# Optimization experiments

Measured on AMD Instinct MI355X. Metric: run time of the kernel, lower is better.

Reference implementation:

```python
import jax, jax.numpy as jnp
import numpy as np

N, E, B = 50000, 800000, 128
F_IN, F_MID, HEADS = 78, 156, 2

def setup_inputs() -> dict:
    key = jax.random.key(0)
    ks = jax.random.split(key, 20)
    s = 0.05
    x = jax.random.normal(ks[0], (N, F_IN), dtype=jnp.float32)
    edge_index = jax.random.randint(ks[1], (2, E), 0, N, dtype=jnp.int64)
    batch = jnp.sort(jax.random.randint(ks[2], (N,), 0, B, dtype=jnp.int64))
    return {
        'x': x, 'edge_index': edge_index, 'batch': batch,
        'W1': jax.random.normal(ks[3], (F_IN, F_MID), jnp.float32) * s,
        'b1': jnp.zeros((F_MID,), jnp.float32),
        'W2': jax.random.normal(ks[4], (F_MID, HEADS * F_MID), jnp.float32) * s,
        'att_src': jax.random.normal(ks[5], (HEADS, F_MID), jnp.float32) * s,
        'att_dst': jax.random.normal(ks[6], (HEADS, F_MID), jnp.float32) * s,
        'b2': jnp.zeros((HEADS * F_MID,), jnp.float32),
        'Wg': jax.random.normal(ks[7], (HEADS * F_MID, 128), jnp.float32) * s,
        'bg': jnp.zeros((128,), jnp.float32),
        'Wf1': jax.random.normal(ks[8], (128, 1024), jnp.float32) * s,
        'bf1': jnp.zeros((1024,), jnp.float32),
        'Wf2': jax.random.normal(ks[9], (1024, 512), jnp.float32) * s,
        'bf2': jnp.zeros((512,), jnp.float32),
        'Wo': jax.random.normal(ks[10], (512, 1), jnp.float32) * s,
        'bo': jnp.zeros((1,), jnp.float32),
    }

def _forward(x, edge_index, batch, W1, b1, W2, att_src, att_dst, b2,
             Wg, bg, Wf1, bf1, Wf2, bf2, Wo, bo):
    n = x.shape[0]
    loop = jnp.arange(n, dtype=edge_index.dtype)
    src = jnp.concatenate([edge_index[0], loop])  # with self-loops (PyG default)
    dst = jnp.concatenate([edge_index[1], loop])

    # ---- GCNConv: D^{-1/2}(A+I)D^{-1/2} X W + b ----
    h = x @ W1                                            # [N,156]
    deg = jax.ops.segment_sum(jnp.ones_like(dst, jnp.float32), dst, num_segments=n)
    dinv = jnp.where(deg > 0, jax.lax.rsqrt(jnp.maximum(deg, 1.0)), 0.0)
    norm = dinv[src] * dinv[dst]                          # [E+N]
    h = jax.ops.segment_sum(h[src] * norm[:, None], dst, num_segments=n) + b1
    h = jax.nn.leaky_relu(h, 0.01)                        # self.activation

    # ---- GATConv (heads=2, concat) ----
    g = (h @ W2).reshape(n, HEADS, F_MID)                 # [N,H,F]
    a_src = jnp.einsum('nhf,hf->nh', g, att_src)          # [N,H]
    a_dst = jnp.einsum('nhf,hf->nh', g, att_dst)
    e = jax.nn.leaky_relu(a_src[src] + a_dst[dst], 0.2)   # [E+N,H]
    m = jax.ops.segment_max(e, dst, num_segments=n)       # per-dst softmax
    alpha = jnp.exp(e - m[dst])
    denom = jax.ops.segment_sum(alpha, dst, num_segments=n)
    alpha = alpha / denom[dst]
    g = jax.ops.segment_sum(g[src] * alpha[:, :, None], dst, num_segments=n)
    g = g.reshape(n, HEADS * F_MID) + b2
    g = jax.nn.leaky_relu(g, 0.01)

    # ---- global max pool over graphs ----
    p = jax.ops.segment_max(g, batch, num_segments=B)     # [B,312]

    p = jax.nn.leaky_relu(p @ Wg + bg, 0.01)              # fc_g1 + activation
    p = jax.nn.relu(p @ Wf1 + bf1)                        # fc1
    p = jax.nn.relu(p @ Wf2 + bf2)                        # fc2
    return p @ Wo + bo                                    # out [B,1]

def reference(x, edge_index, batch, W1, b1, W2, att_src, att_dst, b2,
              Wg, bg, Wf1, bf1, Wf2, bf2, Wo, bo):
    return _forward(x, edge_index, batch, W1, b1, W2, att_src, att_dst, b2,
                    Wg, bg, Wf1, bf1, Wf2, bf2, Wo, bo)
```

## Files before the change

kernel.cpp:

```cpp
#include <hip/hip_runtime.h>
#include <cstdint>
#include <cstddef>

#define F_INP 78
#define F_MID 156
#define C2    312
#define GDIM  128
#define F1D   1024
#define F2D   512

#define NEG_SENTINEL -1e30f
#define SCAN_BLOCKS 256

typedef _Float16 half_t;
typedef _Float16 half8 __attribute__((ext_vector_type(8)));
typedef float f32x4 __attribute__((ext_vector_type(4)));

__device__ __forceinline__ float leaky(float v, float s) { return v > 0.f ? v : s * v; }
__device__ __forceinline__ int rfl(int v) { return __builtin_amdgcn_readfirstlane(v); }


__global__ void deg_count_kernel(const int* __restrict__ ei, int* __restrict__ deg, int E) {
    int e = blockIdx.x * blockDim.x + threadIdx.x;
    if (e >= E) return;
    atomicAdd(&deg[ei[E + e]], 1);
}

__global__ void scan_p1_kernel(const int* __restrict__ deg, int* __restrict__ partials, int N) {
    __shared__ int red[256];
    int b = blockIdx.x, t = threadIdx.x;
    int chunk = (N + SCAN_BLOCKS - 1) / SCAN_BLOCKS;
    int start = b * chunk;
    int end = start + chunk; if (end > N) end = N;
    int s = 0;
    for (int i = start + t; i < end; i += 256) s += deg[i];
    red[t] = s;
    __syncthreads();
    for (int off = 128; off; off >>= 1) {
        if (t < off) red[t] += red[t + off];
        __syncthreads();
    }
    if (t == 0) partials[b] = red[0];
}

__global__ void scan_p2_kernel(int* __restrict__ partials) {
    __shared__ int s[SCAN_BLOCKS];
    int t = threadIdx.x;
    s[t] = partials[t];
    __syncthreads();
    for (int off = 1; off < SCAN_BLOCKS; off <<= 1) {
        int v = (t >= off) ? s[t - off] : 0;
        __syncthreads();
        s[t] += v;
        __syncthreads();
    }
    partials[t] = (t == 0) ? 0 : s[t - 1];
}

__global__ void scan_p3_kernel(const int* __restrict__ deg, const int* __restrict__ partials,
                               int* __restrict__ row_ptr, int* __restrict__ cursor,
                               float* __restrict__ dinv, int N, int E) {
    __shared__ int red[256];
    int b = blockIdx.x, t = threadIdx.x;
    int chunk = (N + SCAN_BLOCKS - 1) / SCAN_BLOCKS;
    int start = b * chunk;
    int end = start + chunk; if (end > N) end = N;
    int sub = (chunk + 255) / 256;
    int ts = start + t * sub;
    int te = ts + sub; if (te > end) te = end; if (ts > end) ts = end;
    int s = 0;
    for (int i = ts; i < te; i++) s += deg[i];
    red[t] = s;
    __syncthreads();
    for (int off = 1; off < 256; off <<= 1) {
        int v = (t >= off) ? red[t - off] : 0;
        __syncthreads();
        red[t] += v;
        __syncthreads();
    }
    int run = partials[b] + ((t == 0) ? 0 : red[t - 1]);
    for (int i = ts; i < te; i++) {
        int dg = deg[i];
        row_ptr[i] = run;
        cursor[i] = run;
        dinv[i] = rsqrtf((float)dg + 1.0f);
        run += dg;
    }
    if (b == 0 && t == 0) row_ptr[N] = E;
}

__global__ void fill_csr_kernel(const int* __restrict__ ei, int* __restrict__ cursor,
                                int* __restrict__ col, int E) {
    int e = blockIdx.x * blockDim.x + threadIdx.x;
    if (e >= E) return;
    int s = ei[e], d = ei[E + e];
    int pos = atomicAdd(&cursor[d], 1);
    col[pos] = s;
}


__global__ void lin1_kernel(const float* __restrict__ x, const float* __restrict__ W1,
                            const float* __restrict__ dinv, half_t* __restrict__ h_lin, int N) {
    __shared__ float2 xs[16][39];
    int tid = threadIdx.x;
    int n0 = blockIdx.x * 16;
    const float2* x2 = (const float2*)x;
    for (int i = tid; i < 16 * 39; i += 192) {
        int r = i / 39, c = i % 39;
        int n = n0 + r;
        float2 z; z.x = 0.f; z.y = 0.f;
        if (n < N) {
            float dn = dinv[n];
            float2 v = x2[(size_t)n * 39 + c];
            z.x = v.x * dn; z.y = v.y * dn;
        }
        xs[r][c] = z;
    }
    __syncthreads();
    if (tid >= 160) return;
    if (tid >= F_MID) {
        for (int r = 0; r < 16; r++) {
            int n = n0 + r;
            if (n < N) h_lin[(size_t)n * 160 + tid] = (half_t)0.f;
        }
        return;
    }
    float acc[16] = {};
    for (int k2 = 0; k2 < 39; k2++) {
        float w0 = W1[(2 * k2) * F_MID + tid];
        float w1 = W1[(2 * k2 + 1) * F_MID + tid];
        #pragma unroll
        for (int r = 0; r < 16; r++) {
            float2 xv = xs[r][k2];
            acc[r] += xv.x * w0 + xv.y * w1;
        }
    }
    #pragma unroll
    for (int r = 0; r < 16; r++) {
        int n = n0 + r;
        if (n < N) h_lin[(size_t)n * 160 + tid] = (half_t)acc[r];
    }
}

__global__ void w2t_kernel(const float* __restrict__ W2, half_t* __restrict__ w2t) {
    int idx = blockIdx.x * blockDim.x + threadIdx.x;
    if (idx >= 320 * 160) return;
    int coln = idx / 160, k = idx % 160;
    float v = (coln < C2 && k < F_MID) ? W2[k * C2 + coln] : 0.f;
    w2t[idx] = (half_t)v;
}

__global__ void wT_kernel(const float* __restrict__ Wg, const float* __restrict__ Wf1,
                          const float* __restrict__ Wf2, float* __restrict__ wgT,
                          float* __restrict__ wf1T, float* __restrict__ wf2T) {
    int idx = blockIdx.x * blockDim.x + threadIdx.x;
    if (idx < GDIM * C2) {
        int c = idx / C2, k = idx % C2;
        wgT[idx] = Wg[k * GDIM + c];
        return;
    }
    idx -= GDIM * C2;
    if (idx < F1D * GDIM) {
        int c = idx / GDIM, k = idx % GDIM;
        wf1T[idx] = Wf1[k * F1D + c];
        return;
    }
    idx -= F1D * GDIM;
    if (idx < F2D * F1D) {
        int c = idx / F1D, k = idx % F1D;
        wf2T[idx] = Wf2[k * F2D + c];
    }
}

__global__ void lin2_mfma_kernel(const half_t* __restrict__ h16, const half_t* __restrict__ w2t,
                                 half_t* __restrict__ g, int N) {
    int wid  = (blockIdx.x * blockDim.x + threadIdx.x) >> 6;
    int lane = threadIdx.x & 63;
    int m0 = wid * 32;
    if (m0 >= N) return;
    int rl = lane & 15;
    int kg = lane >> 4;
    bool has2 = (m0 + 16) < N;

    const half8* hv = (const half8*)h16;
    const half8* wv = (const half8*)w2t;
    half8 zz = {(half_t)0.f,(half_t)0.f,(half_t)0.f,(half_t)0.f,
                (half_t)0.f,(half_t)0.f,(half_t)0.f,(half_t)0.f};

    half8 a0[5], a1[5];
    size_t rA = (size_t)(m0 + rl) * 20;
    size_t rB = (size_t)(m0 + 16 + rl) * 20;
    #pragma unroll
    for (int ks = 0; ks < 5; ks++) {
        a0[ks] = hv[rA + ks * 4 + kg];
        a1[ks] = has2 ? hv[rB + ks * 4 + kg] : zz;
    }

    for (int n0 = 0; n0 < 20; n0++) {
        f32x4 c0 = {0.f, 0.f, 0.f, 0.f};
        f32x4 c1 = {0.f, 0.f, 0.f, 0.f};
        size_t wb = (size_t)(n0 * 16 + rl) * 20 + kg;
        #pragma unroll
        for (int ks = 0; ks < 5; ks++) {
            half8 b = wv[wb + ks * 4];
            c0 = __builtin_amdgcn_mfma_f32_16x16x32_f16(a0[ks], b, c0, 0, 0, 0);
            c1 = __builtin_amdgcn_mfma_f32_16x16x32_f16(a1[ks], b, c1, 0, 0, 0);
        }
        int col = n0 * 16 + rl;
        if (col < C2) {
            int r0 = kg * 4;
            #pragma unroll
            for (int j = 0; j < 4; j++) {
                g[(size_t)(m0 + r0 + j) * C2 + col] = (half_t)c0[j];
            }
            if (has2) {
                #pragma unroll
                for (int j = 0; j < 4; j++) {
                    g[(size_t)(m0 + 16 + r0 + j) * C2 + col] = (half_t)c1[j];
                }
            }
        }
    }
}

__global__ void gcn_gather_kernel(const half_t* __restrict__ h_lin, const int* __restrict__ row_ptr,
                                  const int* __restrict__ col, const float* __restrict__ dinv,
                                  const float* __restrict__ b1, half_t* __restrict__ h16, int N) {
    int wid  = (blockIdx.x * blockDim.x + threadIdx.x) >> 6;
    int lane = threadIdx.x & 63;
    if (wid >= N) return;
    int d  = wid;
    int jb = row_ptr[d], je = row_ptr[d + 1];
    float dd = dinv[d];
    const half8* h8v = (const half8*)h_lin;
    bool actv = lane < 20;
    int f0 = lane * 8;
    float acc[8] = {};
    if (actv) {
        half8 v = h8v[(size_t)d * 20 + lane];
        #pragma unroll
        for (int e = 0; e < 8; e++) acc[e] = (float)v[e];
    }
    int j = jb;
    for (; j + 3 < je; j += 4) {
        int s0 = rfl(col[j]);
        int s1 = rfl(col[j + 1]);
        int s2 = rfl(col[j + 2]);
        int s3 = rfl(col[j + 3]);
        if (actv) {
            half8 v0 = h8v[(size_t)s0 * 20 + lane];
            half8 v1 = h8v[(size_t)s1 * 20 + lane];
            half8 v2 = h8v[(size_t)s2 * 20 + lane];
            half8 v3 = h8v[(size_t)s3 * 20 + lane];
            #pragma unroll
            for (int e = 0; e < 8; e++)
                acc[e] += (float)v0[e] + (float)v1[e] + (float)v2[e] + (float)v3[e];
        }
    }
    for (; j < je; j++) {
        int s = rfl(col[j]);
        if (actv) {
            half8 v = h8v[(size_t)s * 20 + lane];
            #pragma unroll
            for (int e = 0; e < 8; e++) acc[e] += (float)v[e];
        }
    }
    if (actv) {
        half8 o;
        #pragma unroll
        for (int e = 0; e < 8; e++) {
            int f = f0 + e;
            float val = 0.f;
            if (f < F_MID) val = leaky(dd * acc[e] + b1[f], 0.01f);
            o[e] = (half_t)val;
        }
        ((half8*)h16)[(size_t)d * 20 + lane] = o;
    }
}

__global__ void att_kernel(const half_t* __restrict__ g, const float* __restrict__ att_src,
                           const float* __restrict__ att_dst, float2* __restrict__ a_src,
                           float2* __restrict__ a_dst, int N) {
    int wid  = (blockIdx.x * blockDim.x + threadIdx.x) >> 6;
    int lane = threadIdx.x & 63;
    if (wid >= N) return;
    const half8* g8 = (const half8*)g;
    float vs0 = 0.f, vs1 = 0.f, vd0 = 0.f, vd1 = 0.f;
    if (lane < 39) {
        half8 v = g8[(size_t)wid * 39 + lane];
        int f0 = lane * 8;
        #pragma unroll
        for (int e = 0; e < 8; e++) {
            int f = f0 + e;
            float gv = (float)v[e];
            float sw = att_src[f];
            float dw = att_dst[f];
            if (f < F_MID) { vs0 += gv * sw; vd0 += gv * dw; }
            else           { vs1 += gv * sw; vd1 += gv * dw; }
        }
    }
    #pragma unroll
    for (int off = 32; off; off >>= 1) {
        vs0 += __shfl_xor(vs0, off);
        vs1 += __shfl_xor(vs1, off);
        vd0 += __shfl_xor(vd0, off);
        vd1 += __shfl_xor(vd1, off);
    }
    if (lane == 0) {
        float2 s; s.x = vs0; s.y = vs1;
        float2 t; t.x = vd0; t.y = vd1;
        a_src[wid] = s;
        a_dst[wid] = t;
    }
}

__global__ void gat_msw_kernel(const float2* __restrict__ a_src, const float2* __restrict__ a_dst,
                               const int* __restrict__ row_ptr, const int* __restrict__ col,
                               float4* __restrict__ minv, float2* __restrict__ wbuf, int N) {
    int wid  = (blockIdx.x * blockDim.x + threadIdx.x) >> 6;
    int lane = threadIdx.x & 63;
    if (wid >= N) return;
    int d  = wid;
    int jb = row_ptr[d], je = row_ptr[d + 1];
    float2 ad = a_dst[d];
    float2 asd = a_src[d];
    float es0 = leaky(asd.x + ad.x, 0.2f);
    float es1 = leaky(asd.y + ad.y, 0.2f);

    float m0 = NEG_SENTINEL, s0 = 0.f, m1 = NEG_SENTINEL, s1 = 0.f;
    for (int j = jb + lane; j < je; j += 64) {
        float2 as = a_src[col[j]];
        float e0 = leaky(as.x + ad.x, 0.2f);
        float e1 = leaky(as.y + ad.y, 0.2f);
        float nm0 = fmaxf(m0, e0); s0 = s0 * __expf(m0 - nm0) + __expf(e0 - nm0); m0 = nm0;
        float nm1 = fmaxf(m1, e1); s1 = s1 * __expf(m1 - nm1) + __expf(e1 - nm1); m1 = nm1;
    }
    #pragma unroll
    for (int off = 32; off; off >>= 1) {
        float om0 = __shfl_xor(m0, off), os0 = __shfl_xor(s0, off);
        float om1 = __shfl_xor(m1, off), os1 = __shfl_xor(s1, off);
        float nm0 = fmaxf(m0, om0);
        s0 = s0 * __expf(m0 - nm0) + os0 * __expf(om0 - nm0); m0 = nm0;
        float nm1 = fmaxf(m1, om1);
        s1 = s1 * __expf(m1 - nm1) + os1 * __expf(om1 - nm1); m1 = nm1;
    }
    {
        float nm0 = fmaxf(m0, es0);
        s0 = s0 * __expf(m0 - nm0) + __expf(es0 - nm0); m0 = nm0;
        float nm1 = fmaxf(m1, es1);
        s1 = s1 * __expf(m1 - nm1) + __expf(es1 - nm1); m1 = nm1;
    }
    float i0 = 1.0f / s0, i1 = 1.0f / s1;
    if (lane == 0) {
        float4 r; r.x = m0; r.y = i0; r.z = m1; r.w = i1;
        minv[d] = r;
    }
    for (int j = jb + lane; j < je; j += 64) {
        float2 as = a_src[col[j]];
        float2 w;
        w.x = __expf(leaky(as.x + ad.x, 0.2f) - m0) * i0;
        w.y = __expf(leaky(as.y + ad.y, 0.2f) - m1) * i1;
        wbuf[j] = w;
    }
}

__global__ void gat_gather_kernel(const half_t* __restrict__ g, const float2* __restrict__ a_src,
                                  const float2* __restrict__ a_dst, const int* __restrict__ row_ptr,
                                  const int* __restrict__ col, const float2* __restrict__ wbuf,
                                  const float4* __restrict__ minv, float* __restrict__ gout, int N) {
    int wid  = (blockIdx.x * blockDim.x + threadIdx.x) >> 6;
    int lane = threadIdx.x & 63;
    if (wid >= N) return;
    int d  = wid;
    int jb = row_ptr[d], je = row_ptr[d + 1];
    const half8* g8 = (const half8*)g;
    bool actv = lane < 39;
    int f0 = lane * 8;
    bool lo0 = f0 < F_MID;
    bool hi0 = (f0 + 4) < F_MID;
    float acc[8] = {};
    {
        float2 ad = a_dst[d];
        float2 asd = a_src[d];
        float4 mv = minv[d];
        float w0 = __expf(leaky(asd.x + ad.x, 0.2f) - mv.x) * mv.y;
        float w1 = __expf(leaky(asd.y + ad.y, 0.2f) - mv.z) * mv.w;
        if (actv) {
            half8 v = g8[(size_t)d * 39 + lane];
            float wlo = lo0 ? w0 : w1;
            float whi = hi0 ? w0 : w1;
            #pragma unroll
            for (int e = 0; e < 4; e++) acc[e] = (float)v[e] * wlo;
            #pragma unroll
            for (int e = 4; e < 8; e++) acc[e] = (float)v[e] * whi;
        }
    }
    int j = jb;
    for (; j + 3 < je; j += 4) {
        int s0 = rfl(col[j]);
        int s1 = rfl(col[j + 1]);
        int s2 = rfl(col[j + 2]);
        int s3 = rfl(col[j + 3]);
        float2 W0 = wbuf[j], W1v = wbuf[j + 1], W2v = wbuf[j + 2], W3v = wbuf[j + 3];
        if (actv) {
            half8 v0 = g8[(size_t)s0 * 39 + lane];
            half8 v1 = g8[(size_t)s1 * 39 + lane];
            half8 v2 = g8[(size_t)s2 * 39 + lane];
            half8 v3 = g8[(size_t)s3 * 39 + lane];
            float a0 = lo0 ? W0.x : W0.y,  b0 = hi0 ? W0.x : W0.y;
            float a1 = lo0 ? W1v.x : W1v.y, b1 = hi0 ? W1v.x : W1v.y;
            float a2 = lo0 ? W2v.x : W2v.y, b2 = hi0 ? W2v.x : W2v.y;
            float a3 = lo0 ? W3v.x : W3v.y, b3 = hi0 ? W3v.x : W3v.y;
            #pragma unroll
            for (int e = 0; e < 4; e++)
                acc[e] += (float)v0[e] * a0 + (float)v1[e] * a1 + (float)v2[e] * a2 + (float)v3[e] * a3;
            #pragma unroll
            for (int e = 4; e < 8; e++)
                acc[e] += (float)v0[e] * b0 + (float)v1[e] * b1 + (float)v2[e] * b2 + (float)v3[e] * b3;
        }
    }
    for (; j < je; j++) {
        int s = rfl(col[j]);
        float2 w2 = wbuf[j];
        if (actv) {
            half8 v = g8[(size_t)s * 39 + lane];
            float wlo = lo0 ? w2.x : w2.y;
            float whi = hi0 ? w2.x : w2.y;
            #pragma unroll
            for (int e = 0; e < 4; e++) acc[e] += (float)v[e] * wlo;
            #pragma unroll
            for (int e = 4; e < 8; e++) acc[e] += (float)v[e] * whi;
        }
    }
    if (actv) {
        float* orow = gout + (size_t)d * C2 + f0;
        float4 o0; o0.x = acc[0]; o0.y = acc[1]; o0.z = acc[2]; o0.w = acc[3];
        float4 o1; o1.x = acc[4]; o1.y = acc[5]; o1.z = acc[6]; o1.w = acc[7];
        *(float4*)orow = o0;
        *(float4*)(orow + 4) = o1;
    }
}


__global__ void starts_kernel(const int* __restrict__ batch, int* __restrict__ starts, int N, int B) {
    int b = blockIdx.x * blockDim.x + threadIdx.x;
    if (b > B) return;
    if (b == B) { starts[B] = N; return; }
    int lo = 0, hi = N;
    while (lo < hi) {
        int mid = (lo + hi) >> 1;
        if (batch[mid] < b) lo = mid + 1; else hi = mid;
    }
    starts[b] = lo;
}

__global__ void pool_kernel(const float* __restrict__ gout, const float* __restrict__ b2,
                            const int* __restrict__ starts, float* __restrict__ p0) {
    int b = blockIdx.x;
    int t = threadIdx.x;
    if (t >= 78) return;
    int s = starts[b], e = starts[b + 1];
    const float4* g4 = (const float4*)gout;
    float4 m0, m1, m2, m3;
    m0.x = m0.y = m0.z = m0.w = -INFINITY;
    m1 = m0; m2 = m0; m3 = m0;
    int n = s;
    for (; n + 3 < e; n += 4) {
        float4 v0 = g4[(size_t)(n + 0) * 78 + t];
        float4 v1 = g4[(size_t)(n + 1) * 78 + t];
        float4 v2 = g4[(size_t)(n + 2) * 78 + t];
        float4 v3 = g4[(size_t)(n + 3) * 78 + t];
        m0.x = fmaxf(m0.x, v0.x); m0.y = fmaxf(m0.y, v0.y); m0.z = fmaxf(m0.z, v0.z); m0.w = fmaxf(m0.w, v0.w);
        m1.x = fmaxf(m1.x, v1.x); m1.y = fmaxf(m1.y, v1.y); m1.z = fmaxf(m1.z, v1.z); m1.w = fmaxf(m1.w, v1.w);
        m2.x = fmaxf(m2.x, v2.x); m2.y = fmaxf(m2.y, v2.y); m2.z = fmaxf(m2.z, v2.z); m2.w = fmaxf(m2.w, v2.w);
        m3.x = fmaxf(m3.x, v3.x); m3.y = fmaxf(m3.y, v3.y); m3.z = fmaxf(m3.z, v3.z); m3.w = fmaxf(m3.w, v3.w);
    }
    for (; n < e; n++) {
        float4 v = g4[(size_t)n * 78 + t];
        m0.x = fmaxf(m0.x, v.x); m0.y = fmaxf(m0.y, v.y); m0.z = fmaxf(m0.z, v.z); m0.w = fmaxf(m0.w, v.w);
    }
    m0.x = fmaxf(fmaxf(m0.x, m1.x), fmaxf(m2.x, m3.x));
    m0.y = fmaxf(fmaxf(m0.y, m1.y), fmaxf(m2.y, m3.y));
    m0.z = fmaxf(fmaxf(m0.z, m1.z), fmaxf(m2.z, m3.z));
    m0.w = fmaxf(fmaxf(m0.w, m1.w), fmaxf(m2.w, m3.w));
    float4 bb = ((const float4*)b2)[t];
    float4 o;
    o.x = leaky(m0.x + bb.x, 0.01f);
    o.y = leaky(m0.y + bb.y, 0.01f);
    o.z = leaky(m0.z + bb.z, 0.01f);
    o.w = leaky(m0.w + bb.w, 0.01f);
    ((float4*)p0)[(size_t)b * 78 + t] = o;
}

template <int KDIM, int ACT>
__global__ void fcT_kernel(const float* __restrict__ in, const float* __restrict__ Wt,
                           const float* __restrict__ bias, float* __restrict__ out,
                           int Bn, int OUT) {
    int wid  = (blockIdx.x * blockDim.x + threadIdx.x) >> 6;
    int lane = threadIdx.x & 63;
    if (wid >= Bn * OUT) return;
    int b = wid / OUT, c = wid % OUT;
    const float* irow = in + (size_t)b * KDIM;
    const float* wrow = Wt + (size_t)c * KDIM;
    float acc = 0.f;
    #pragma unroll 4
    for (int k = lane; k < KDIM; k += 64)
        acc += irow[k] * wrow[k];
    #pragma unroll
    for (int off = 32; off; off >>= 1) acc += __shfl_xor(acc, off);
    if (lane == 0) {
        acc += bias[c];
        if (ACT == 1) acc = leaky(acc, 0.01f);
        if (ACT == 2) acc = fmaxf(acc, 0.f);
        out[wid] = acc;
    }
}

extern "C" void kernel_launch(void* const* d_in, const int* in_sizes, int n_in,
                              void* d_out, int out_size, void* d_ws, size_t ws_size,
                              hipStream_t stream) {
    const float* x       = (const float*)d_in[0];
    const int*   ei      = (const int*)d_in[1];
    const int*   batch   = (const int*)d_in[2];
    const float* W1      = (const float*)d_in[3];
    const float* b1      = (const float*)d_in[4];
    const float* W2      = (const float*)d_in[5];
    const float* att_src = (const float*)d_in[6];
    const float* att_dst = (const float*)d_in[7];
    const float* b2      = (const float*)d_in[8];
    const float* Wg      = (const float*)d_in[9];
    const float* bg      = (const float*)d_in[10];
    const float* Wf1     = (const float*)d_in[11];
    const float* bf1     = (const float*)d_in[12];
    const float* Wf2     = (const float*)d_in[13];
    const float* bf2     = (const float*)d_in[14];
    const float* Wo      = (const float*)d_in[15];
    const float* bo      = (const float*)d_in[16];
    float* out = (float*)d_out;

    const int N  = in_sizes[0] / F_INP;
    const int E  = in_sizes[1] / 2;
    const int Bn = out_size;

    char* base = (char*)d_ws;
    size_t off = 0;
    auto take = [&](size_t bytes) -> void* {
        off = (off + 15) & ~(size_t)15;
        void* p = base + off;
        off += bytes;
        return p;
    };
    half_t* g      = (half_t*)take((size_t)C2 * N * 2);
    char*   AA     = (char*)take((size_t)C2 * N * 4);
    half_t* h_lin  = (half_t*)AA;
    half_t* h16    = (half_t*)(AA + (size_t)160 * N * 2);
    float*  gout   = (float*)AA;
    half_t* w2t    = (half_t*)take((size_t)320 * 160 * 2);
    float*  wgT    = (float*)take((size_t)GDIM * C2 * 4);
    float*  wf1T   = (float*)take((size_t)F1D * GDIM * 4);
    float*  wf2T   = (float*)take((size_t)F2D * F1D * 4);
    float4* minv   = (float4*)take((size_t)N * 16);
    float2* a_src  = (float2*)take((size_t)N * 8);
    float2* a_dst  = (float2*)take((size_t)N * 8);
    float2* wbuf   = (float2*)take((size_t)E * 8);
    float*  dinv   = (float*)take((size_t)N * 4);
    int*    deg_i  = (int*)take((size_t)N * 4);
    int*    partials = (int*)take((size_t)SCAN_BLOCKS * 4);
    int*    row_ptr= (int*)take((size_t)(N + 1) * 4);
    int*    cursor = (int*)take((size_t)N * 4);
    int*    col    = (int*)take((size_t)E * 4);
    int*    starts = (int*)take((size_t)(Bn + 1) * 4);
    float*  p0     = (float*)take((size_t)Bn * C2 * 4);
    float*  p1     = (float*)take((size_t)Bn * GDIM * 4);
    float*  p2     = (float*)take((size_t)Bn * F1D * 4);
    float*  p3     = (float*)take((size_t)Bn * F2D * 4);

    hipMemsetAsync(deg_i, 0, (size_t)N * sizeof(int), stream);

    starts_kernel<<<1, 256, 0, stream>>>(batch, starts, N, Bn);
    w2t_kernel<<<(320 * 160 + 255) / 256, 256, 0, stream>>>(W2, w2t);
    {
        int tot = GDIM * C2 + F1D * GDIM + F2D * F1D;
        wT_kernel<<<(tot + 255) / 256, 256, 0, stream>>>(Wg, Wf1, Wf2, wgT, wf1T, wf2T);
    }

    deg_count_kernel<<<(E + 255) / 256, 256, 0, stream>>>(ei, deg_i, E);
    scan_p1_kernel<<<SCAN_BLOCKS, 256, 0, stream>>>(deg_i, partials, N);
    scan_p2_kernel<<<1, SCAN_BLOCKS, 0, stream>>>(partials);
    scan_p3_kernel<<<SCAN_BLOCKS, 256, 0, stream>>>(deg_i, partials, row_ptr, cursor, dinv, N, E);
    fill_csr_kernel<<<(E + 255) / 256, 256, 0, stream>>>(ei, cursor, col, E);

    lin1_kernel<<<(N + 15) / 16, 192, 0, stream>>>(x, W1, dinv, h_lin, N);
    gcn_gather_kernel<<<(N + 3) / 4, 256, 0, stream>>>(h_lin, row_ptr, col, dinv, b1, h16, N);

    {
        int mwaves = (N + 31) / 32;
        int blocks = (mwaves + 3) / 4;
        lin2_mfma_kernel<<<blocks, 256, 0, stream>>>(h16, w2t, g, N);
    }
    att_kernel<<<(N + 3) / 4, 256, 0, stream>>>(g, att_src, att_dst, a_src, a_dst, N);
    gat_msw_kernel<<<(N + 3) / 4, 256, 0, stream>>>(a_src, a_dst, row_ptr, col, minv, wbuf, N);
    gat_gather_kernel<<<(N + 3) / 4, 256, 0, stream>>>(g, a_src, a_dst, row_ptr, col, wbuf, minv, gout, N);

    pool_kernel<<<Bn, 128, 0, stream>>>(gout, b2, starts, p0);
    {
        auto blocks_for = [](int waves) { return (waves + 3) / 4; };
        fcT_kernel<C2, 1><<<blocks_for(Bn * GDIM), 256, 0, stream>>>(p0, wgT, bg, p1, Bn, GDIM);
        fcT_kernel<GDIM, 2><<<blocks_for(Bn * F1D), 256, 0, stream>>>(p1, wf1T, bf1, p2, Bn, F1D);
        fcT_kernel<F1D, 2><<<blocks_for(Bn * F2D), 256, 0, stream>>>(p2, wf2T, bf2, p3, Bn, F2D);
        fcT_kernel<F2D, 0><<<blocks_for(Bn), 256, 0, stream>>>(p3, Wo, bo, out, Bn, 1);
    }
}
```

Measured before the change: 537.8 us.

## Use MFMA for first linear layer and store GAT output in fp16

Replaces the scalar fp32 lin1 kernel with a pre-pass that scales x by dinv and converts it to padded fp16, a transposed fp16 W1, and an MFMA 16x16x32 GEMM. Separately, the GAT gather output is now written as fp16 instead of fp32, and the pooling kernel reads half8 vectors, halving the traffic between those two kernels. In exchange it adds two extra launches and reduced precision in x and the pooled input. The MFMA kernel reads rows up to m0+31 of hx without a full tail guard, which could run out of bounds when N is not a multiple of 32; N=50000 is a multiple of 16 but not of 32.

Result: faster. 508.2 us (-5.5%).

```diff
diff --git a/kernel.cpp b/kernel.cpp
--- a/kernel.cpp
+++ b/kernel.cpp
@@ -99,46 +99,75 @@
 }
 
 
-__global__ void lin1_kernel(const float* __restrict__ x, const float* __restrict__ W1,
-                            const float* __restrict__ dinv, half_t* __restrict__ h_lin, int N) {
-    __shared__ float2 xs[16][39];
-    int tid = threadIdx.x;
-    int n0 = blockIdx.x * 16;
-    const float2* x2 = (const float2*)x;
-    for (int i = tid; i < 16 * 39; i += 192) {
-        int r = i / 39, c = i % 39;
-        int n = n0 + r;
-        float2 z; z.x = 0.f; z.y = 0.f;
-        if (n < N) {
-            float dn = dinv[n];
-            float2 v = x2[(size_t)n * 39 + c];
-            z.x = v.x * dn; z.y = v.y * dn;
-        }
-        xs[r][c] = z;
-    }
-    __syncthreads();
-    if (tid >= 160) return;
-    if (tid >= F_MID) {
-        for (int r = 0; r < 16; r++) {
-            int n = n0 + r;
-            if (n < N) h_lin[(size_t)n * 160 + tid] = (half_t)0.f;
-        }
-        return;
-    }
-    float acc[16] = {};
-    for (int k2 = 0; k2 < 39; k2++) {
-        float w0 = W1[(2 * k2) * F_MID + tid];
-        float w1 = W1[(2 * k2 + 1) * F_MID + tid];
-        #pragma unroll
-        for (int r = 0; r < 16; r++) {
-            float2 xv = xs[r][k2];
-            acc[r] += xv.x * w0 + xv.y * w1;
-        }
-    }
-    #pragma unroll
-    for (int r = 0; r < 16; r++) {
-        int n = n0 + r;
-        if (n < N) h_lin[(size_t)n * 160 + tid] = (half_t)acc[r];
+__global__ void x16_kernel(const float* __restrict__ x, const float* __restrict__ dinv,
+                           half_t* __restrict__ hx, int N) {
+    int idx = blockIdx.x * blockDim.x + threadIdx.x;
+    if (idx >= N * 12) return;
+    int n = idx / 12, c = idx % 12;
+    float dn = dinv[n];
+    half8 o;
+    int k0 = c * 8;
+    #pragma unroll
+    for (int e = 0; e < 8; e++) {
+        int k = k0 + e;
+        float v = (k < F_INP) ? x[(size_t)n * F_INP + k] * dn : 0.f;
+        o[e] = (half_t)v;
+    }
+    ((half8*)hx)[idx] = o;
+}
+
+__global__ void w1t_kernel(const float* __restrict__ W1, half_t* __restrict__ w1t) {
+    int idx = blockIdx.x * blockDim.x + threadIdx.x;
+    if (idx >= 160 * 96) return;
+    int c = idx / 96, k = idx % 96;
+    float v = (c < F_MID && k < F_INP) ? W1[k * F_MID + c] : 0.f;
+    w1t[idx] = (half_t)v;
+}
+
+__global__ void lin1_mfma_kernel(const half_t* __restrict__ hx, const half_t* __restrict__ w1t,
+                                 half_t* __restrict__ h_lin, int N) {
+    int wid  = (blockIdx.x * blockDim.x + threadIdx.x) >> 6;
+    int lane = threadIdx.x & 63;
+    int m0 = wid * 32;
+    if (m0 >= N) return;
+    int rl = lane & 15;
+    int kg = lane >> 4;
+    bool has2 = (m0 + 16) < N;
+
+    const half8* hv = (const half8*)hx;
+    const half8* wv = (const half8*)w1t;
+    half8 zz = {(half_t)0.f,(half_t)0.f,(half_t)0.f,(half_t)0.f,
+                (half_t)0.f,(half_t)0.f,(half_t)0.f,(half_t)0.f};
+
+    half8 a0[3], a1[3];
+    size_t rA = (size_t)(m0 + rl) * 12;
+    size_t rB = (size_t)(m0 + 16 + rl) * 12;
+    #pragma unroll
+    for (int ks = 0; ks < 3; ks++) {
+        a0[ks] = hv[rA + ks * 4 + kg];
+        a1[ks] = has2 ? hv[rB + ks * 4 + kg] : zz;
+    }
+
+    for (int n0 = 0; n0 < 10; n0++) {
+        f32x4 c0 = {0.f, 0.f, 0.f, 0.f};
+        f32x4 c1 = {0.f, 0.f, 0.f, 0.f};
+        size_t wb = (size_t)(n0 * 16 + rl) * 12 + kg;
+        #pragma unroll
+        for (int ks = 0; ks < 3; ks++) {
+            half8 b = wv[wb + ks * 4];
+            c0 = __builtin_amdgcn_mfma_f32_16x16x32_f16(a0[ks], b, c0, 0, 0, 0);
+            c1 = __builtin_amdgcn_mfma_f32_16x16x32_f16(a1[ks], b, c1, 0, 0, 0);
+        }
+        int col = n0 * 16 + rl;
+        int r0 = kg * 4;
+        #pragma unroll
+        for (int j = 0; j < 4; j++)
+            h_lin[(size_t)(m0 + r0 + j) * 160 + col] = (half_t)c0[j];
+        if (has2) {
+            #pragma unroll
+            for (int j = 0; j < 4; j++)
+                h_lin[(size_t)(m0 + 16 + r0 + j) * 160 + col] = (half_t)c1[j];
+        }
     }
 }
 
@@ -367,7 +396,7 @@
 __global__ void gat_gather_kernel(const half_t* __restrict__ g, const float2* __restrict__ a_src,
                                   const float2* __restrict__ a_dst, const int* __restrict__ row_ptr,
                                   const int* __restrict__ col, const float2* __restrict__ wbuf,
-                                  const float4* __restrict__ minv, float* __restrict__ gout, int N) {
+                                  const float4* __restrict__ minv, half_t* __restrict__ gout, int N) {
     int wid  = (blockIdx.x * blockDim.x + threadIdx.x) >> 6;
     int lane = threadIdx.x & 63;
     if (wid >= N) return;
@@ -433,11 +462,10 @@
         }
     }
     if (actv) {
-        float* orow = gout + (size_t)d * C2 + f0;
-        float4 o0; o0.x = acc[0]; o0.y = acc[1]; o0.z = acc[2]; o0.w = acc[3];
-        float4 o1; o1.x = acc[4]; o1.y = acc[5]; o1.z = acc[6]; o1.w = acc[7];
-        *(float4*)orow = o0;
-        *(float4*)(orow + 4) = o1;
+        half8 o;
+        #pragma unroll
+        for (int e = 0; e < 8; e++) o[e] = (half_t)acc[e];
+        ((half8*)gout)[(size_t)d * 39 + lane] = o;
     }
 }
 
@@ -454,42 +482,39 @@
     starts[b] = lo;
 }
 
-__global__ void pool_kernel(const float* __restrict__ gout, const float* __restrict__ b2,
+__global__ void pool_kernel(const half_t* __restrict__ gout, const float* __restrict__ b2,
                             const int* __restrict__ starts, float* __restrict__ p0) {
     int b = blockIdx.x;
     int t = threadIdx.x;
-    if (t >= 78) return;
+    if (t >= 39) return;
     int s = starts[b], e = starts[b + 1];
-    const float4* g4 = (const float4*)gout;
-    float4 m0, m1, m2, m3;
-    m0.x = m0.y = m0.z = m0.w = -INFINITY;
-    m1 = m0; m2 = m0; m3 = m0;
+    const half8* g8 = (const half8*)gout;
+    float m[8];
+    #pragma unroll
+    for (int i = 0; i < 8; i++) m[i] = -INFINITY;
     int n = s;
     for (; n + 3 < e; n += 4) {
-        float4 v0 = g4[(size_t)(n + 0) * 78 + t];
-        float4 v1 = g4[(size_t)(n + 1) * 78 + t];
-        float4 v2 = g4[(size_t)(n + 2) * 78 + t];
-        float4 v3 = g4[(size_t)(n + 3) * 78 + t];
-        m0.x = fmaxf(m0.x, v0.x); m0.y = fmaxf(m0.y, v0.y); m0.z = fmaxf(m0.z, v0.z); m0.w = fmaxf(m0.w, v0.w);
-        m1.x = fmaxf(m1.x, v1.x); m1.y = fmaxf(m1.y, v1.y); m1.z = fmaxf(m1.z, v1.z); m1.w = fmaxf(m1.w, v1.w);
-        m2.x = fmaxf(m2.x, v2.x); m2.y = fmaxf(m2.y, v2.y); m2.z = fmaxf(m2.z, v2.z); m2.w = fmaxf(m2.w, v2.w);
-        m3.x = fmaxf(m3.x, v3.x); m3.y = fmaxf(m3.y, v3.y); m3.z = fmaxf(m3.z, v3.z); m3.w = fmaxf(m3.w, v3.w);
+        half8 v0 = g8[(size_t)(n + 0) * 39 + t];
+        half8 v1 = g8[(size_t)(n + 1) * 39 + t];
+        half8 v2 = g8[(size_t)(n + 2) * 39 + t];
+        half8 v3 = g8[(size_t)(n + 3) * 39 + t];
+        #pragma unroll
+        for (int i = 0; i < 8; i++) {
+            float a = fmaxf((float)v0[i], (float)v1[i]);
+            float c = fmaxf((float)v2[i], (float)v3[i]);
+            m[i] = fmaxf(m[i], fmaxf(a, c));
+        }
     }
     for (; n < e; n++) {
-        float4 v = g4[(size_t)n * 78 + t];
-        m0.x = fmaxf(m0.x, v.x); m0.y = fmaxf(m0.y, v.y); m0.z = fmaxf(m0.z, v.z); m0.w = fmaxf(m0.w, v.w);
-    }
-    m0.x = fmaxf(fmaxf(m0.x, m1.x), fmaxf(m2.x, m3.x));
-    m0.y = fmaxf(fmaxf(m0.y, m1.y), fmaxf(m2.y, m3.y));
-    m0.z = fmaxf(fmaxf(m0.z, m1.z), fmaxf(m2.z, m3.z));
-    m0.w = fmaxf(fmaxf(m0.w, m1.w), fmaxf(m2.w, m3.w));
-    float4 bb = ((const float4*)b2)[t];
-    float4 o;
-    o.x = leaky(m0.x + bb.x, 0.01f);
-    o.y = leaky(m0.y + bb.y, 0.01f);
-    o.z = leaky(m0.z + bb.z, 0.01f);
-    o.w = leaky(m0.w + bb.w, 0.01f);
-    ((float4*)p0)[(size_t)b * 78 + t] = o;
+        half8 v = g8[(size_t)n * 39 + t];
+        #pragma unroll
+        for (int i = 0; i < 8; i++) m[i] = fmaxf(m[i], (float)v[i]);
+    }
+    int f0 = t * 8;
+    float* orow = p0 + (size_t)b * C2 + f0;
+    #pragma unroll
+    for (int i = 0; i < 8; i++)
+        orow[i] = leaky(m[i] + b2[f0 + i], 0.01f);
 }
 
 template <int KDIM, int ACT>
@@ -554,7 +579,9 @@
     char*   AA     = (char*)take((size_t)C2 * N * 4);
     half_t* h_lin  = (half_t*)AA;
     half_t* h16    = (half_t*)(AA + (size_t)160 * N * 2);
-    float*  gout   = (float*)AA;
+    half_t* gout   = (half_t*)AA;
+    half_t* hx     = (half_t*)take((size_t)96 * N * 2);
+    half_t* w1t    = (half_t*)take((size_t)160 * 96 * 2);
     half_t* w2t    = (half_t*)take((size_t)320 * 160 * 2);
     float*  wgT    = (float*)take((size_t)GDIM * C2 * 4);
     float*  wf1T   = (float*)take((size_t)F1D * GDIM * 4);
@@ -578,6 +605,7 @@
     hipMemsetAsync(deg_i, 0, (size_t)N * sizeof(int), stream);
 
     starts_kernel<<<1, 256, 0, stream>>>(batch, starts, N, Bn);
+    w1t_kernel<<<(160 * 96 + 255) / 256, 256, 0, stream>>>(W1, w1t);
     w2t_kernel<<<(320 * 160 + 255) / 256, 256, 0, stream>>>(W2, w2t);
     {
         int tot = GDIM * C2 + F1D * GDIM + F2D * F1D;
@@ -590,19 +618,22 @@
     scan_p3_kernel<<<SCAN_BLOCKS, 256, 0, stream>>>(deg_i, partials, row_ptr, cursor, dinv, N, E);
     fill_csr_kernel<<<(E + 255) / 256, 256, 0, stream>>>(ei, cursor, col, E);
 
-    lin1_kernel<<<(N + 15) / 16, 192, 0, stream>>>(x, W1, dinv, h_lin, N);
-    gcn_gather_kernel<<<(N + 3) / 4, 256, 0, stream>>>(h_lin, row_ptr, col, dinv, b1, h16, N);
-
+    x16_kernel<<<(N * 12 + 255) / 256, 256, 0, stream>>>(x, dinv, hx, N);
     {
         int mwaves = (N + 31) / 32;
-        int blocks = (mwaves + 3) / 4;
-        lin2_mfma_kernel<<<blocks, 256, 0, stream>>>(h16, w2t, g, N);
+        lin1_mfma_kernel<<<(mwaves + 3) / 4, 256, 0, stream>>>(hx, w1t, h_lin, N);
+    }
+    gcn_gather_kernel<<<(N + 3) / 4, 256, 0, stream>>>(h_lin, row_ptr, col, dinv, b1, h16, N);
+
+    {
+        int mwaves = (N + 31) / 32;
+        lin2_mfma_kernel<<<(mwaves + 3) / 4, 256, 0, stream>>>(h16, w2t, g, N);
     }
     att_kernel<<<(N + 3) / 4, 256, 0, stream>>>(g, att_src, att_dst, a_src, a_dst, N);
     gat_msw_kernel<<<(N + 3) / 4, 256, 0, stream>>>(a_src, a_dst, row_ptr, col, minv, wbuf, N);
     gat_gather_kernel<<<(N + 3) / 4, 256, 0, stream>>>(g, a_src, a_dst, row_ptr, col, wbuf, minv, gout, N);
 
-    pool_kernel<<<Bn, 128, 0, stream>>>(gout, b2, starts, p0);
+    pool_kernel<<<Bn, 64, 0, stream>>>(gout, b2, starts, p0);
     {
         auto blocks_for = [](int waves) { return (waves + 3) / 4; };
         fcT_kernel<C2, 1><<<blocks_for(Bn * GDIM), 256, 0, stream>>>(p0, wgT, bg, p1, Bn, GDIM);
```
